# Kernel optimization log

Measured on AMD Instinct MI355X. Metric: run time of the kernel, lower is better.

Reference implementation:

```python
import jax, jax.numpy as jnp
import numpy as np

N_TOKENS = 100000
CUT = [0, 20000, 50000, 100000]  # cutoff_ends
D = 1024


def setup_inputs() -> dict:
    key = jax.random.key(0)
    ks = jax.random.split(key, 12)
    B, S = 2, 1024
    hidden = jax.random.normal(ks[0], (B, S, D), dtype=jnp.float32)
    target = jax.random.randint(ks[1], (B, S), 0, N_TOKENS, dtype=jnp.int64)
    s = 0.02
    # cluster 0 (shortlist) + cluster projection head
    w0 = jax.random.normal(ks[2], (20000, 1024), dtype=jnp.float32) * s
    b0 = jnp.zeros((20000,), jnp.float32)
    cluster_w = jax.random.normal(ks[3], (2, 1024), dtype=jnp.float32) * s  # n_clusters=2
    cluster_b = jnp.zeros((2,), jnp.float32)
    proj0 = jax.random.normal(ks[4], (1024, 1024), dtype=jnp.float32) * s  # d_proj x d_emb_0
    # tail cluster 1: d_emb_1 = 1024 // 4 = 256, vocab slice 20000..50000
    w1 = jax.random.normal(ks[5], (30000, 256), dtype=jnp.float32) * s
    b1 = jnp.zeros((30000,), jnp.float32)
    proj1 = jax.random.normal(ks[6], (1024, 256), dtype=jnp.float32) * s
    # tail cluster 2: d_emb_2 = 1024 // 16 = 64, vocab slice 50000..100000
    w2 = jax.random.normal(ks[7], (50000, 64), dtype=jnp.float32) * s
    b2 = jnp.zeros((50000,), jnp.float32)
    proj2 = jax.random.normal(ks[8], (1024, 64), dtype=jnp.float32) * s
    return {"hidden": hidden, "target": target,
            "w0": w0, "b0": b0, "cluster_w": cluster_w, "cluster_b": cluster_b, "proj0": proj0,
            "w1": w1, "b1": b1, "proj1": proj1,
            "w2": w2, "b2": b2, "proj2": proj2}


def reference(hidden, target, w0, b0, cluster_w, cluster_b, proj0,
              w1, b1, proj1, w2, b2, proj2):
    tgt_shape = target.shape
    h = hidden.reshape(-1, D)            # [N, d_proj]
    t = target.reshape(-1)               # [N]

    # head: shortlist logits + cluster logits, via low-rank projection
    head_w = jnp.concatenate([w0, cluster_w], axis=0)   # [20002, 1024]
    head_b = jnp.concatenate([b0, cluster_b], axis=0)
    head_logit = (h @ proj0) @ head_w.T + head_b        # [N, 20002]
    head_lp = jax.nn.log_softmax(head_logit, axis=1)

    nll = jnp.zeros(t.shape, h.dtype)

    # cluster 0 (shortlist): logprob is head_lp at the target id
    m0 = t < CUT[1]
    idx0 = jnp.clip(t, 0, CUT[1] - 1)
    lp0 = jnp.take_along_axis(head_lp, idx0[:, None], axis=1)[:, 0]
    nll = jnp.where(m0, -lp0, nll)

    # tail clusters. NOTE: faithful to original quirk head_logprob[:, -i]
    tails = [(CUT[1], CUT[2], w1, b1, proj1), (CUT[2], CUT[3], w2, b2, proj2)]
    for i, (left, right, w, b, p) in enumerate(tails, start=1):
        m = (t >= left) & (t < right)
        tail_logit = (h @ p) @ w.T + b                  # [N, right-left]
        tail_lp = jax.nn.log_softmax(tail_logit, axis=1)
        ti = jnp.clip(t - left, 0, right - left - 1)
        lp = head_lp[:, -i] + jnp.take_along_axis(tail_lp, ti[:, None], axis=1)[:, 0]
        nll = jnp.where(m, -lp, nll)

    return nll.reshape(tgt_shape)
```

## Files before the change

### kernel.cpp

```cpp
#include <hip/hip_runtime.h>
#include <cstdint>
#include <cstddef>

#define DEV static __device__ __forceinline__

typedef __attribute__((ext_vector_type(8))) short bf16x8_t;
typedef __attribute__((ext_vector_type(4))) float f32x4_t;

DEV unsigned short f2bf(float f) {
  union { float f; unsigned u; } v; v.f = f;
  unsigned r = v.u + 0x7fffu + ((v.u >> 16) & 1u);
  return (unsigned short)(r >> 16);
}

DEV void gl_lds16(const void* g, void* l) {
  __builtin_amdgcn_global_load_lds(
      (const __attribute__((address_space(1))) void*)g,
      (__attribute__((address_space(3))) void*)l,
      16, 0, 0);
}

__global__ __launch_bounds__(256)
void prep_k(const int* __restrict__ target,
            int* __restrict__ idx1, int* __restrict__ pos1,
            int* __restrict__ idx2, int* __restrict__ pos2,
            int* __restrict__ cnts,
            const float* __restrict__ p0, const float* __restrict__ p1,
            const float* __restrict__ p2, unsigned short* __restrict__ pAll,
            const float* __restrict__ s0, unsigned short* __restrict__ d0, int n0,
            const float* __restrict__ s1, unsigned short* __restrict__ d1, int n1,
            const float* __restrict__ s2, unsigned short* __restrict__ d2, int n2,
            const float* __restrict__ s3, unsigned short* __restrict__ d3, int n3,
            const float* __restrict__ s4, unsigned short* __restrict__ d4, int n4) {
  const int bid = blockIdx.x;
  const int tid = threadIdx.x;
  if (bid == 0) {
    __shared__ int c1, c2;
    if (tid == 0) { c1 = 0; c2 = 0; }
    __syncthreads();
    for (int i = tid; i < 2048; i += 256) {
      int t = target[i];
      if (t >= 20000 && t < 50000) {
        int p = atomicAdd(&c1, 1); idx1[p] = i; pos1[i] = p;
      } else if (t >= 50000) {
        int p = atomicAdd(&c2, 1); idx2[p] = i; pos2[i] = p;
      }
    }
    __syncthreads();
    if (tid == 0) { cnts[0] = c1; cnts[1] = c2; }
    return;
  }
  if (bid <= 1344) {
    __shared__ float tile[32][33];
    int b = bid - 1;
    const float* src; unsigned short* dst; int C, bx, by;
    if (b < 1024)      { src = p0; dst = pAll;               C = 1024; bx = b % 32; by = b / 32; }
    else if (b < 1280) { int q = b - 1024; src = p1; dst = pAll + 1024 * 1024; C = 256; bx = q % 8; by = q / 8; }
    else               { int q = b - 1280; src = p2; dst = pAll + 1280 * 1024; C = 64;  bx = q % 2; by = q / 2; }
    const int R = 1024;
    int tx = tid & 31, ty = tid >> 5;
    int c0 = bx * 32, r0 = by * 32;
    for (int yy = ty; yy < 32; yy += 8)
      tile[yy][tx] = src[(size_t)(r0 + yy) * C + (c0 + tx)];
    __syncthreads();
    for (int yy = ty; yy < 32; yy += 8)
      dst[(size_t)(c0 + yy) * R + (r0 + tx)] = f2bf(tile[tx][yy]);
    return;
  }
  int j = (bid - 1345) * 256 + tid;
  const float* s; unsigned short* d;
  if (j < n0) { s = s0; d = d0; }
  else { j -= n0;
    if (j < n1) { s = s1; d = d1; }
    else { j -= n1;
      if (j < n2) { s = s2; d = d2; }
      else { j -= n2;
        if (j < n3) { s = s3; d = d3; }
        else { j -= n3; if (j >= n4) return; s = s4; d = d4; }
      }
    }
  }
  float4 f = ((const float4*)s)[j];
  ushort4 o;
  o.x = f2bf(f.x); o.y = f2bf(f.y); o.z = f2bf(f.z); o.w = f2bf(f.w);
  ((ushort4*)d)[j] = o;
}

__global__ __launch_bounds__(256)
void proj_gemm_k(const unsigned short* __restrict__ A,
                 const unsigned short* __restrict__ W,
                 unsigned short* __restrict__ Cout) {
  __shared__ __align__(16) unsigned short As[128 * 32];
  __shared__ __align__(16) unsigned short Bs[128 * 32];
  const int K = 1024, V = 1344;
  const int tm = blockIdx.x, tn = blockIdx.y;
  const int m0 = tm * 128, n0 = tn * 128;
  const int tid = threadIdx.x, wid = tid >> 6, lane = tid & 63;
  const int quad = lane >> 4, l16 = lane & 15;
  const int wr = wid >> 1, wc = wid & 1;

  f32x4_t acc[4][4];
  const f32x4_t zero4 = {0.f, 0.f, 0.f, 0.f};
#pragma unroll
  for (int i = 0; i < 4; ++i)
#pragma unroll
    for (int j = 0; j < 4; ++j) acc[i][j] = zero4;

  const int srow = wid * 32 + (lane >> 2);
  const int skk  = (lane & 3) * 8;
  const unsigned short* Ap0 = A + (size_t)(m0 + srow) * K + skk;
  const unsigned short* Ap1 = A + (size_t)(m0 + srow + 16) * K + skk;
  int wrow0 = n0 + srow;      if (wrow0 > V - 1) wrow0 = V - 1;
  int wrow1 = n0 + srow + 16; if (wrow1 > V - 1) wrow1 = V - 1;
  const unsigned short* Wp0 = W + (size_t)wrow0 * K + skk;
  const unsigned short* Wp1 = W + (size_t)wrow1 * K + skk;
  unsigned short* Asw = As + wid * 1024;
  unsigned short* Bsw = Bs + wid * 1024;

  for (int k0 = 0; k0 < K; k0 += 32) {
    gl_lds16(Ap0, Asw);
    gl_lds16(Ap1, Asw + 512);
    gl_lds16(Wp0, Bsw);
    gl_lds16(Wp1, Bsw + 512);
    Ap0 += 32; Ap1 += 32; Wp0 += 32; Wp1 += 32;
    __syncthreads();
    bf16x8_t af[4], bfr[4];
#pragma unroll
    for (int i = 0; i < 4; ++i)
      af[i] = *(const bf16x8_t*)(As + (size_t)(wr * 64 + i * 16 + l16) * 32 + quad * 8);
#pragma unroll
    for (int j = 0; j < 4; ++j)
      bfr[j] = *(const bf16x8_t*)(Bs + (size_t)(wc * 64 + j * 16 + l16) * 32 + quad * 8);
#pragma unroll
    for (int i = 0; i < 4; ++i)
#pragma unroll
      for (int j = 0; j < 4; ++j)
        acc[i][j] = __builtin_amdgcn_mfma_f32_16x16x32_bf16(af[i], bfr[j], acc[i][j], 0, 0, 0);
    __syncthreads();
  }
#pragma unroll
  for (int i = 0; i < 4; ++i)
#pragma unroll
    for (int j = 0; j < 4; ++j) {
      const int n = n0 + wc * 64 + j * 16 + l16;
      if (n < V) {
#pragma unroll
        for (int r = 0; r < 4; ++r) {
          const int m = m0 + wr * 64 + i * 16 + quad * 4 + r;
          Cout[(size_t)m * V + n] = f2bf(acc[i][j][r]);
        }
      }
    }
}


#define SBAR()                                                                \
  __builtin_amdgcn_sched_barrier(0);                                          \
  __builtin_amdgcn_s_barrier();                                               \
  __builtin_amdgcn_sched_barrier(0)

#define LGKM0()                                                               \
  asm volatile("s_waitcnt lgkmcnt(0)" ::: "memory");                          \
  __builtin_amdgcn_sched_barrier(0)

#define STA(BUF, HALF, KT)                                                    \
  {                                                                           \
    const unsigned short* g_ = aB0 + (size_t)(HALF) * (128 * 1344) + (KT) * 64; \
    char* d_ = (char*)SA[BUF][HALF] + ldsw;                                   \
    gl_lds16(g_, d_);                                                         \
    gl_lds16(g_ + 64 * 1344, d_ + 8192);                                      \
  }

#define STB(BUF, HALF, KT)                                                    \
  {                                                                           \
    char* d_ = (char*)SB[BUF][HALF] + ldsw;                                   \
    gl_lds16(bP##HALF##0 + (KT) * 64, d_);                                    \
    gl_lds16(bP##HALF##1 + (KT) * 64, d_ + 8192);                             \
  }

#define MM16(mb, nb)                                                          \
  {                                                                           \
    _Pragma("unroll") for (int mi = 0; mi < 4; ++mi) {                        \
      _Pragma("unroll") for (int nj = 0; nj < 2; ++nj) {                      \
        acc[(mb) + mi][(nb) + nj] = __builtin_amdgcn_mfma_f32_16x16x32_bf16(  \
            Af[0][mi], Bf[(nb) / 2][0][nj], acc[(mb) + mi][(nb) + nj], 0, 0, 0); \
        acc[(mb) + mi][(nb) + nj] = __builtin_amdgcn_mfma_f32_16x16x32_bf16(  \
            Af[1][mi], Bf[(nb) / 2][1][nj], acc[(mb) + mi][(nb) + nj], 0, 0, 0); \
      }                                                                       \
    }                                                                         \
  }

#define PH(D_, E_, KTV)                                                       \
  {                                                                           \
    const int kt_ = (KTV);                                                    \
    const int t1_ = (kt_ + 1 > 15) ? 15 : (kt_ + 1);                          \
    const int t2_ = (kt_ + 2 > 15) ? 15 : (kt_ + 2);                          \
                   \
    _Pragma("unroll") for (int mi = 0; mi < 4; ++mi) {                        \
      Af[0][mi] = *(const bf16x8_t*)(pa##D_##a + mi * 2048);                  \
      Af[1][mi] = *(const bf16x8_t*)(pa##D_##b + mi * 2048);                  \
    }                                                                         \
    _Pragma("unroll") for (int nj = 0; nj < 2; ++nj) {                        \
      Bf[0][0][nj] = *(const bf16x8_t*)(pb##D_##a + nj * 2048);               \
      Bf[0][1][nj] = *(const bf16x8_t*)(pb##D_##b + nj * 2048);               \
    }                                                                         \
    STB(E_, 1, t1_);                                                          \
    SBAR();                                                                   \
    LGKM0();                                                                  \
    __builtin_amdgcn_s_setprio(1);                                            \
    MM16(0, 0);                                                               \
    __builtin_amdgcn_s_setprio(0);                                            \
                                            \
    _Pragma("unroll") for (int nj = 0; nj < 2; ++nj) {                        \
      Bf[1][0][nj] = *(const bf16x8_t*)(pb##D_##a + (2 + nj) * 2048);         \
      Bf[1][1][nj] = *(const bf16x8_t*)(pb##D_##b + (2 + nj) * 2048);         \
    }                                                                         \
    SBAR();                                                                   \
    STA(E_, 1, t1_);                                                          \
    SBAR();                                                                   \
    LGKM0();                                                                  \
    __builtin_amdgcn_s_setprio(1);                                            \
    MM16(0, 2);                                                               \
    __builtin_amdgcn_s_setprio(0);                                            \
       \
    _Pragma("unroll") for (int mi = 0; mi < 4; ++mi) {                        \
      Af[0][mi] = *(const bf16x8_t*)(pa##D_##a + (4 + mi) * 2048);            \
      Af[1][mi] = *(const bf16x8_t*)(pa##D_##b + (4 + mi) * 2048);            \
    }                                                                         \
    SBAR();                                                                   \
    STB(D_, 0, t2_);                                                          \
    SBAR();                                                                   \
    LGKM0();                                                                  \
    __builtin_amdgcn_s_setprio(1);                                            \
    MM16(4, 0);                                                               \
    __builtin_amdgcn_s_setprio(0);                                            \
    SBAR();                                                                   \
    STA(D_, 0, t2_);                                                          \
    SBAR();                                                                   \
    __builtin_amdgcn_s_setprio(1);                                            \
    MM16(4, 2);                                                               \
    __builtin_amdgcn_s_setprio(0);                                            \
    asm volatile("s_waitcnt vmcnt(4)" ::: "memory");                          \
    SBAR();                                                                   \
  }

__global__ __launch_bounds__(512, 2)
void head256_k(const unsigned short* __restrict__ Pall,
               const unsigned short* __restrict__ w0b,
               const float* __restrict__ b0, const float* __restrict__ cb,
               float* __restrict__ part0, float* __restrict__ g0,
               float* __restrict__ cg, const int* __restrict__ target) {
  __shared__ __align__(16) unsigned short SA[2][2][8192];
  __shared__ __align__(16) unsigned short SB[2][2][8192];

  const int V = 20002;
  const int bid = blockIdx.x;
  const int orig = (bid & 7) * 79 + (bid >> 3);
  const int mt = orig & 7, stripe = orig >> 3;
  const int m0 = mt * 256, n0 = stripe * 256;

  const int tid = threadIdx.x;
  const int wid = tid >> 6, lane = tid & 63;
  const int quad = lane >> 4, l16 = lane & 15;
  const int wr = wid >> 2, wc = wid & 3;

  const int r0  = tid >> 3;
  const int ibh = ((tid & 7) ^ (r0 & 7)) << 3;

  const unsigned short* aB0 = Pall + (size_t)(m0 + r0) * 1344 + ibh;
  int br00 = n0 + r0;            if (br00 > V - 1) br00 = V - 1;
  int br01 = n0 + r0 + 64;       if (br01 > V - 1) br01 = V - 1;
  int br10 = n0 + 128 + r0;      if (br10 > V - 1) br10 = V - 1;
  int br11 = n0 + 128 + r0 + 64; if (br11 > V - 1) br11 = V - 1;
  const unsigned short* bP00 = w0b + (size_t)br00 * 1024 + ibh;
  const unsigned short* bP01 = w0b + (size_t)br01 * 1024 + ibh;
  const unsigned short* bP10 = w0b + (size_t)br10 * 1024 + ibh;
  const unsigned short* bP11 = w0b + (size_t)br11 * 1024 + ibh;

  const int ldsw = wid * 1024;

  const int aoff0 = l16 * 128 + ((quad ^ (l16 & 3)) << 4) + (((l16 >> 2) & 1) << 6);
  const int aoff1 = aoff0 ^ 64;
  const char* pa0a = (const char*)SA[0][wr] + aoff0;
  const char* pa0b = (const char*)SA[0][wr] + aoff1;
  const char* pa1a = (const char*)SA[1][wr] + aoff0;
  const char* pa1b = (const char*)SA[1][wr] + aoff1;
  const char* pb0a = (const char*)SB[0][wc >> 1] + (wc & 1) * 8192 + aoff0;
  const char* pb0b = (const char*)SB[0][wc >> 1] + (wc & 1) * 8192 + aoff1;
  const char* pb1a = (const char*)SB[1][wc >> 1] + (wc & 1) * 8192 + aoff0;
  const char* pb1b = (const char*)SB[1][wc >> 1] + (wc & 1) * 8192 + aoff1;

  f32x4_t acc[8][4];
  const f32x4_t zero4 = {0.f, 0.f, 0.f, 0.f};
#pragma unroll
  for (int i = 0; i < 8; ++i)
#pragma unroll
    for (int j = 0; j < 4; ++j) acc[i][j] = zero4;

  bf16x8_t Af[2][4];
  bf16x8_t Bf[2][2][2];

  STB(0, 0, 0); STA(0, 0, 0); STB(0, 1, 0); STA(0, 1, 0);
  STB(1, 0, 1); STA(1, 0, 1);
  asm volatile("s_waitcnt vmcnt(4)" ::: "memory");
  SBAR();

#pragma unroll 1
  for (int ktp = 0; ktp < 8; ++ktp) {
    const int kt0 = 2 * ktp;
    PH(0, 1, kt0);
    PH(1, 0, kt0 + 1);
  }

  asm volatile("s_waitcnt vmcnt(0)" ::: "memory");
  SBAR();

  int nj[4]; float bj[4];
#pragma unroll
  for (int j = 0; j < 4; ++j) {
    nj[j] = n0 + wc * 64 + j * 16 + l16;
    bj[j] = (nj[j] < 20000) ? b0[nj[j]] : ((nj[j] < V) ? cb[nj[j] - 20000] : 0.f);
  }
  float* redf = (float*)&SA[0][0][0];
#pragma unroll
  for (int i = 0; i < 8; ++i) {
#pragma unroll
    for (int r = 0; r < 4; ++r) {
      const int rloc = i * 16 + quad * 4 + r;
      const int token = m0 + wr * 128 + rloc;
      float v[4], sum = 0.f;
#pragma unroll
      for (int j = 0; j < 4; ++j) {
        v[j] = acc[i][j][r] + bj[j];
        if (nj[j] < V) sum += __expf(v[j]);
      }
#pragma unroll
      for (int off = 1; off < 16; off <<= 1)
        sum += __shfl_xor(sum, off, 64);
      if (l16 == 0) redf[(wr * 4 + wc) * 128 + rloc] = sum;
      const int t = target[token];
      const int gi = (t < 19999) ? t : 19999;
#pragma unroll
      for (int j = 0; j < 4; ++j) {
        if (nj[j] == gi) g0[token] = v[j];
        if (nj[j] == 20000) cg[2 * token]     = v[j];
        if (nj[j] == 20001) cg[2 * token + 1] = v[j];
      }
    }
  }
  __syncthreads();
  if (tid < 256) {
    const int wrr = tid >> 7, rr = tid & 127;
    const float s = redf[(wrr * 4 + 0) * 128 + rr] + redf[(wrr * 4 + 1) * 128 + rr]
                  + redf[(wrr * 4 + 2) * 128 + rr] + redf[(wrr * 4 + 3) * 128 + rr];
    part0[(size_t)(m0 + tid) * 79 + stripe] = s;
  }
}

#undef PH
#undef MM16
#undef STA
#undef STB
#undef SBAR
#undef LGKM0

template <int KT>
__global__ __launch_bounds__(256, 1)
void tail_stripe_k(const unsigned short* __restrict__ A, int ldA,
                   const unsigned short* __restrict__ W,
                   const float* __restrict__ bias, int V, int ntiles,
                   const int* __restrict__ rowidx,
                   const int* __restrict__ cnt_ptr,
                   float* __restrict__ partials,
                   float* __restrict__ gathered,
                   const int* __restrict__ target, int glo) {
  constexpr int NC = KT / 32;
  __shared__ __align__(16) unsigned short Ws[NC][128 * 32];
  __shared__ __align__(16) unsigned short As[NC][128 * 32];
  __shared__ float red[2][128];

  const int tn = blockIdx.x, n0 = tn * 128;
  const int Meff = *cnt_ptr;
  const int tid = threadIdx.x, wid = tid >> 6, lane = tid & 63;
  const int quad = lane >> 4, l16 = lane & 15;
  const int wr = wid >> 1, wc = wid & 1;
  const int srow = wid * 32 + (lane >> 2);
  const int skk  = (lane & 3) * 8;

  int wrow0 = n0 + srow;      if (wrow0 > V - 1) wrow0 = V - 1;
  int wrow1 = n0 + srow + 16; if (wrow1 > V - 1) wrow1 = V - 1;
#pragma unroll
  for (int c = 0; c < NC; ++c) {
    gl_lds16(W + (size_t)wrow0 * KT + c * 32 + skk, Ws[c] + wid * 1024);
    gl_lds16(W + (size_t)wrow1 * KT + c * 32 + skk, Ws[c] + wid * 1024 + 512);
  }

  int nj[4]; float bj[4];
#pragma unroll
  for (int j = 0; j < 4; ++j) {
    nj[j] = n0 + wc * 64 + j * 16 + l16;
    bj[j] = (nj[j] < V) ? bias[nj[j]] : 0.f;
  }

  const int nm = (Meff + 127) >> 7;
  for (int m = 0; m < nm; ++m) {
    const int m0 = m * 128;
    int ar0 = m0 + srow;      if (ar0 > Meff - 1) ar0 = Meff - 1;
    int ar1 = m0 + srow + 16; if (ar1 > Meff - 1) ar1 = Meff - 1;
    ar0 = rowidx[ar0]; ar1 = rowidx[ar1];
#pragma unroll
    for (int c = 0; c < NC; ++c) {
      gl_lds16(A + (size_t)ar0 * ldA + c * 32 + skk, As[c] + wid * 1024);
      gl_lds16(A + (size_t)ar1 * ldA + c * 32 + skk, As[c] + wid * 1024 + 512);
    }
    __syncthreads();

    f32x4_t acc[4][4];
    const f32x4_t zero4 = {0.f, 0.f, 0.f, 0.f};
#pragma unroll
    for (int i = 0; i < 4; ++i)
#pragma unroll
      for (int j = 0; j < 4; ++j) acc[i][j] = zero4;
#pragma unroll
    for (int c = 0; c < NC; ++c) {
      bf16x8_t af[4], bfr[4];
#pragma unroll
      for (int i = 0; i < 4; ++i)
        af[i] = *(const bf16x8_t*)(As[c] + (size_t)(wr * 64 + i * 16 + l16) * 32 + quad * 8);
#pragma unroll
      for (int j = 0; j < 4; ++j)
        bfr[j] = *(const bf16x8_t*)(Ws[c] + (size_t)(wc * 64 + j * 16 + l16) * 32 + quad * 8);
#pragma unroll
      for (int i = 0; i < 4; ++i)
#pragma unroll
        for (int j = 0; j < 4; ++j)
          acc[i][j] = __builtin_amdgcn_mfma_f32_16x16x32_bf16(af[i], bfr[j], acc[i][j], 0, 0, 0);
    }

#pragma unroll
    for (int i = 0; i < 4; ++i) {
#pragma unroll
      for (int r = 0; r < 4; ++r) {
        const int row = wr * 64 + i * 16 + quad * 4 + r;
        const int gr = m0 + row;
        const int grc = (gr < Meff) ? gr : (Meff - 1);
        const int token = rowidx[grc];
        float v[4], sum = 0.f;
#pragma unroll
        for (int j = 0; j < 4; ++j) {
          v[j] = acc[i][j][r] + bj[j];
          if (nj[j] < V) sum += __expf(v[j]);
        }
#pragma unroll
        for (int off = 1; off < 16; off <<= 1)
          sum += __shfl_xor(sum, off, 64);
        if (l16 == 0) red[wc][row] = sum;
        const int gi = target[token] - glo;
#pragma unroll
        for (int j = 0; j < 4; ++j)
          if (nj[j] == gi) gathered[token] = v[j];
      }
    }
    __syncthreads();
    if (tid < 128 && (m0 + tid) < Meff)
      partials[(size_t)(m0 + tid) * ntiles + tn] = red[0][tid] + red[1][tid];
  }
}

__global__ __launch_bounds__(256)
void combine_k(const float* __restrict__ part0,
               const float* __restrict__ part1, int nt1,
               const float* __restrict__ part2, int nt2,
               const float* __restrict__ g0, const float* __restrict__ g1,
               const float* __restrict__ g2, const float* __restrict__ cg,
               const int* __restrict__ pos1, const int* __restrict__ pos2,
               const int* __restrict__ target, float* __restrict__ out) {
  const int w = threadIdx.x >> 6, lane = threadIdx.x & 63;
  const int token = blockIdx.x * 4 + w;
  const int t = target[token];

  float S = 0.f;
  for (int i = lane; i < 79; i += 64)
    S += part0[(size_t)token * 79 + i];
#pragma unroll
  for (int off = 1; off < 64; off <<= 1)
    S += __shfl_xor(S, off, 64);
  const float lse_head = __logf(S);

  float res;
  if (t < 20000) {
    res = lse_head - g0[token];
  } else {
    const float* pt; int nt; float gv, ch; int row;
    if (t < 50000) { pt = part1; nt = nt1; gv = g1[token]; ch = cg[2 * token + 1]; row = pos1[token]; }
    else           { pt = part2; nt = nt2; gv = g2[token]; ch = cg[2 * token];     row = pos2[token]; }
    float S2 = 0.f;
    for (int i = lane; i < nt; i += 64)
      S2 += pt[(size_t)row * nt + i];
#pragma unroll
    for (int off = 1; off < 64; off <<= 1)
      S2 += __shfl_xor(S2, off, 64);
    float lse_t = __logf(S2);
    res = -((ch - lse_head) + (gv - lse_t));
  }
  if (lane == 0) out[token] = res;
}

extern "C" void kernel_launch(void* const* d_in, const int* in_sizes, int n_in,
                              void* d_out, int out_size, void* d_ws, size_t ws_size,
                              hipStream_t stream) {
  (void)in_sizes; (void)n_in; (void)out_size; (void)ws_size;
  const float* hidden = (const float*)d_in[0];
  const int*   target = (const int*)d_in[1];
  const float* w0     = (const float*)d_in[2];
  const float* b0     = (const float*)d_in[3];
  const float* cw     = (const float*)d_in[4];
  const float* cb     = (const float*)d_in[5];
  const float* proj0  = (const float*)d_in[6];
  const float* w1     = (const float*)d_in[7];
  const float* b1     = (const float*)d_in[8];
  const float* proj1  = (const float*)d_in[9];
  const float* w2     = (const float*)d_in[10];
  const float* b2     = (const float*)d_in[11];
  const float* proj2  = (const float*)d_in[12];
  float* out = (float*)d_out;

  const int NT1 = 235, NT2 = 391;

  char* p = (char*)d_ws;
  auto alloc = [&](size_t bytes) {
    char* r = p; p += (bytes + 255) & ~(size_t)255; return r;
  };
  unsigned short* Hb   = (unsigned short*)alloc(2048ull * 1024 * 2);
  unsigned short* pAll = (unsigned short*)alloc(1344ull * 1024 * 2);
  unsigned short* w0b  = (unsigned short*)alloc(20002ull * 1024 * 2);
  unsigned short* w1b  = (unsigned short*)alloc(30000ull * 256 * 2);
  unsigned short* w2b  = (unsigned short*)alloc(50000ull * 64 * 2);
  unsigned short* Pall = (unsigned short*)alloc(2048ull * 1344 * 2);
  float* part0 = (float*)alloc(2048ull * 79 * 4);
  float* part1 = (float*)alloc(2048ull * NT1 * 4);
  float* part2 = (float*)alloc(2048ull * NT2 * 4);
  float* g0 = (float*)alloc(2048 * 4);
  float* g1 = (float*)alloc(2048 * 4);
  float* g2 = (float*)alloc(2048 * 4);
  float* cg = (float*)alloc(2048 * 2 * 4);
  int* idx1 = (int*)alloc(2048 * 4);
  int* pos1 = (int*)alloc(2048 * 4);
  int* idx2 = (int*)alloc(2048 * 4);
  int* pos2 = (int*)alloc(2048 * 4);
  int* cnts = (int*)alloc(2 * 4);

  const int c_h = 2048 * 1024 / 4, c_w0 = 20000 * 1024 / 4, c_cw = 2048 / 4,
            c_w1 = 30000 * 256 / 4, c_w2 = 50000 * 64 / 4;
  const int ctot = c_h + c_w0 + c_cw + c_w1 + c_w2;
  const int nb_cast = (ctot + 255) / 256;
  prep_k<<<1 + 1344 + nb_cast, 256, 0, stream>>>(
      target, idx1, pos1, idx2, pos2, cnts,
      proj0, proj1, proj2, pAll,
      hidden, Hb, c_h,
      w0, w0b, c_w0,
      cw, w0b + 20000ull * 1024, c_cw,
      w1, w1b, c_w1,
      w2, w2b, c_w2);

  proj_gemm_k<<<dim3(16, 11), 256, 0, stream>>>(Hb, pAll, Pall);

  head256_k<<<632, 512, 0, stream>>>(Pall, w0b, b0, cb, part0, g0, cg, target);

  tail_stripe_k<256><<<NT1, 256, 0, stream>>>(
      Pall + 1024, 1344, w1b, b1, 30000, NT1, idx1, cnts + 0,
      part1, g1, target, 20000);
  tail_stripe_k<64><<<NT2, 256, 0, stream>>>(
      Pall + 1280, 1344, w2b, b2, 50000, NT2, idx2, cnts + 1,
      part2, g2, target, 50000);

  combine_k<<<512, 256, 0, stream>>>(part0, part1, NT1, part2, NT2,
      g0, g1, g2, cg, pos1, pos2, target, out);
}
```

Baseline: 428.4 us.

## Make head GEMM persistent with atomic tile scheduler and prefetch-overlapped epilogue

```diff
diff --git a/kernel.cpp b/kernel.cpp
--- a/kernel.cpp
+++ b/kernel.cpp
@@ -47,7 +47,7 @@
       }
     }
     __syncthreads();
-    if (tid == 0) { cnts[0] = c1; cnts[1] = c2; }
+    if (tid == 0) { cnts[0] = c1; cnts[1] = c2; cnts[2] = 256; }
     return;
   }
   if (bid <= 1344) {
@@ -154,14 +154,8 @@
 }
 
 
-#define SBAR()                                                                \
-  __builtin_amdgcn_sched_barrier(0);                                          \
-  __builtin_amdgcn_s_barrier();                                               \
-  __builtin_amdgcn_sched_barrier(0)
-
-#define LGKM0()                                                               \
-  asm volatile("s_waitcnt lgkmcnt(0)" ::: "memory");                          \
-  __builtin_amdgcn_sched_barrier(0)
+#define SBAR() __builtin_amdgcn_s_barrier()
+#define LGKM0() asm volatile("s_waitcnt lgkmcnt(0)" ::: "memory")
 
 #define STA(BUF, HALF, KT)                                                    \
   {                                                                           \
@@ -195,7 +189,7 @@
     const int kt_ = (KTV);                                                    \
     const int t1_ = (kt_ + 1 > 15) ? 15 : (kt_ + 1);                          \
     const int t2_ = (kt_ + 2 > 15) ? 15 : (kt_ + 2);                          \
-                   \
+                                       \
     _Pragma("unroll") for (int mi = 0; mi < 4; ++mi) {                        \
       Af[0][mi] = *(const bf16x8_t*)(pa##D_##a + mi * 2048);                  \
       Af[1][mi] = *(const bf16x8_t*)(pa##D_##b + mi * 2048);                  \
@@ -205,60 +199,52 @@
       Bf[0][1][nj] = *(const bf16x8_t*)(pb##D_##b + nj * 2048);               \
     }                                                                         \
     STB(E_, 1, t1_);                                                          \
+    SBAR(); LGKM0();                                                          \
+    __builtin_amdgcn_s_setprio(1); MM16(0, 0); __builtin_amdgcn_s_setprio(0); \
     SBAR();                                                                   \
-    LGKM0();                                                                  \
-    __builtin_amdgcn_s_setprio(1);                                            \
-    MM16(0, 0);                                                               \
-    __builtin_amdgcn_s_setprio(0);                                            \
-                                            \
+                                               \
     _Pragma("unroll") for (int nj = 0; nj < 2; ++nj) {                        \
       Bf[1][0][nj] = *(const bf16x8_t*)(pb##D_##a + (2 + nj) * 2048);         \
       Bf[1][1][nj] = *(const bf16x8_t*)(pb##D_##b + (2 + nj) * 2048);         \
     }                                                                         \
+    STA(E_, 1, t1_);                                                          \
+    SBAR(); LGKM0();                                                          \
+    __builtin_amdgcn_s_setprio(1); MM16(0, 2); __builtin_amdgcn_s_setprio(0); \
     SBAR();                                                                   \
-    STA(E_, 1, t1_);                                                          \
-    SBAR();                                                                   \
-    LGKM0();                                                                  \
-    __builtin_amdgcn_s_setprio(1);                                            \
-    MM16(0, 2);                                                               \
-    __builtin_amdgcn_s_setprio(0);                                            \
-       \
+                                               \
     _Pragma("unroll") for (int mi = 0; mi < 4; ++mi) {                        \
       Af[0][mi] = *(const bf16x8_t*)(pa##D_##a + (4 + mi) * 2048);            \
       Af[1][mi] = *(const bf16x8_t*)(pa##D_##b + (4 + mi) * 2048);            \
     }                                                                         \
+    STB(D_, 0, t2_);                                                          \
+    SBAR(); LGKM0();                                                          \
+    __builtin_amdgcn_s_setprio(1); MM16(4, 0); __builtin_amdgcn_s_setprio(0); \
     SBAR();                                                                   \
-    STB(D_, 0, t2_);                                                          \
-    SBAR();                                                                   \
-    LGKM0();                                                                  \
-    __builtin_amdgcn_s_setprio(1);                                            \
-    MM16(4, 0);                                                               \
-    __builtin_amdgcn_s_setprio(0);                                            \
-    SBAR();                                                                   \
+                    \
     STA(D_, 0, t2_);                                                          \
     SBAR();                                                                   \
-    __builtin_amdgcn_s_setprio(1);                                            \
-    MM16(4, 2);                                                               \
-    __builtin_amdgcn_s_setprio(0);                                            \
+    __builtin_amdgcn_s_setprio(1); MM16(4, 2); __builtin_amdgcn_s_setprio(0); \
     asm volatile("s_waitcnt vmcnt(4)" ::: "memory");                          \
     SBAR();                                                                   \
   }
+
+#define PROLOGUE6()                                                           \
+  { STB(0, 0, 0); STA(0, 0, 0); STB(0, 1, 0); STA(0, 1, 0);                   \
+    STB(1, 0, 1); STA(1, 0, 1); }
 
 __global__ __launch_bounds__(512, 2)
 void head256_k(const unsigned short* __restrict__ Pall,
                const unsigned short* __restrict__ w0b,
                const float* __restrict__ b0, const float* __restrict__ cb,
                float* __restrict__ part0, float* __restrict__ g0,
-               float* __restrict__ cg, const int* __restrict__ target) {
+               float* __restrict__ cg, const int* __restrict__ target,
+               int* __restrict__ tilectr) {
   __shared__ __align__(16) unsigned short SA[2][2][8192];
   __shared__ __align__(16) unsigned short SB[2][2][8192];
-
-  const int V = 20002;
-  const int bid = blockIdx.x;
-  const int orig = (bid & 7) * 79 + (bid >> 3);
-  const int mt = orig & 7, stripe = orig >> 3;
-  const int m0 = mt * 256, n0 = stripe * 256;
-
+  __shared__ float redf2[1024];
+  __shared__ int nextS;
+
+  const int V = 20002, NTILE = 632;
   const int tid = threadIdx.x;
   const int wid = tid >> 6, lane = tid & 63;
   const int quad = lane >> 4, l16 = lane & 15;
@@ -266,17 +252,6 @@
 
   const int r0  = tid >> 3;
   const int ibh = ((tid & 7) ^ (r0 & 7)) << 3;
-
-  const unsigned short* aB0 = Pall + (size_t)(m0 + r0) * 1344 + ibh;
-  int br00 = n0 + r0;            if (br00 > V - 1) br00 = V - 1;
-  int br01 = n0 + r0 + 64;       if (br01 > V - 1) br01 = V - 1;
-  int br10 = n0 + 128 + r0;      if (br10 > V - 1) br10 = V - 1;
-  int br11 = n0 + 128 + r0 + 64; if (br11 > V - 1) br11 = V - 1;
-  const unsigned short* bP00 = w0b + (size_t)br00 * 1024 + ibh;
-  const unsigned short* bP01 = w0b + (size_t)br01 * 1024 + ibh;
-  const unsigned short* bP10 = w0b + (size_t)br10 * 1024 + ibh;
-  const unsigned short* bP11 = w0b + (size_t)br11 * 1024 + ibh;
-
   const int ldsw = wid * 1024;
 
   const int aoff0 = l16 * 128 + ((quad ^ (l16 & 3)) << 4) + (((l16 >> 2) & 1) << 6);
@@ -290,77 +265,116 @@
   const char* pb1a = (const char*)SB[1][wc >> 1] + (wc & 1) * 8192 + aoff0;
   const char* pb1b = (const char*)SB[1][wc >> 1] + (wc & 1) * 8192 + aoff1;
 
+  int m0, n0, stripe;
+  const unsigned short* aB0;
+  const unsigned short *bP00, *bP01, *bP10, *bP11;
+
+  int tile = blockIdx.x;
+#define DECODE(T)                                                             \
+  {                                                                           \
+    const int t_ = (T);                                                       \
+    stripe = t_ >> 3; m0 = (t_ & 7) * 256; n0 = stripe * 256;                 \
+    aB0 = Pall + (size_t)(m0 + r0) * 1344 + ibh;                              \
+    int q00 = n0 + r0;            if (q00 > V - 1) q00 = V - 1;               \
+    int q01 = n0 + r0 + 64;       if (q01 > V - 1) q01 = V - 1;               \
+    int q10 = n0 + 128 + r0;      if (q10 > V - 1) q10 = V - 1;               \
+    int q11 = n0 + 128 + r0 + 64; if (q11 > V - 1) q11 = V - 1;               \
+    bP00 = w0b + (size_t)q00 * 1024 + ibh;                                    \
+    bP01 = w0b + (size_t)q01 * 1024 + ibh;                                    \
+    bP10 = w0b + (size_t)q10 * 1024 + ibh;                                    \
+    bP11 = w0b + (size_t)q11 * 1024 + ibh;                                    \
+  }
+
+  DECODE(tile);
+  PROLOGUE6();
+  asm volatile("s_waitcnt vmcnt(4)" ::: "memory");
+  SBAR();
+
   f32x4_t acc[8][4];
-  const f32x4_t zero4 = {0.f, 0.f, 0.f, 0.f};
-#pragma unroll
-  for (int i = 0; i < 8; ++i)
-#pragma unroll
-    for (int j = 0; j < 4; ++j) acc[i][j] = zero4;
-
   bf16x8_t Af[2][4];
   bf16x8_t Bf[2][2][2];
-
-  STB(0, 0, 0); STA(0, 0, 0); STB(0, 1, 0); STA(0, 1, 0);
-  STB(1, 0, 1); STA(1, 0, 1);
-  asm volatile("s_waitcnt vmcnt(4)" ::: "memory");
-  SBAR();
+  const f32x4_t zero4 = {0.f, 0.f, 0.f, 0.f};
+
+  while (true) {
+#pragma unroll
+    for (int i = 0; i < 8; ++i)
+#pragma unroll
+      for (int j = 0; j < 4; ++j) acc[i][j] = zero4;
 
 #pragma unroll 1
-  for (int ktp = 0; ktp < 8; ++ktp) {
-    const int kt0 = 2 * ktp;
-    PH(0, 1, kt0);
-    PH(1, 0, kt0 + 1);
-  }
-
-  asm volatile("s_waitcnt vmcnt(0)" ::: "memory");
-  SBAR();
-
-  int nj[4]; float bj[4];
-#pragma unroll
-  for (int j = 0; j < 4; ++j) {
-    nj[j] = n0 + wc * 64 + j * 16 + l16;
-    bj[j] = (nj[j] < 20000) ? b0[nj[j]] : ((nj[j] < V) ? cb[nj[j] - 20000] : 0.f);
-  }
-  float* redf = (float*)&SA[0][0][0];
-#pragma unroll
-  for (int i = 0; i < 8; ++i) {
-#pragma unroll
-    for (int r = 0; r < 4; ++r) {
-      const int rloc = i * 16 + quad * 4 + r;
-      const int token = m0 + wr * 128 + rloc;
-      float v[4], sum = 0.f;
-#pragma unroll
-      for (int j = 0; j < 4; ++j) {
-        v[j] = acc[i][j][r] + bj[j];
-        if (nj[j] < V) sum += __expf(v[j]);
+    for (int ktp = 0; ktp < 8; ++ktp) {
+      const int kt0 = 2 * ktp;
+      PH(0, 1, kt0);
+      PH(1, 0, kt0 + 1);
+    }
+
+    if (tid == 0) nextS = atomicAdd(tilectr, 1);
+    asm volatile("s_waitcnt vmcnt(0) lgkmcnt(0)" ::: "memory");
+    SBAR();
+    const int next = nextS;
+    const bool more = (next < NTILE);
+
+    const int em0 = m0, estripe = stripe;
+    int nj[4]; float bj[4];
+#pragma unroll
+    for (int j = 0; j < 4; ++j) {
+      nj[j] = n0 + wc * 64 + j * 16 + l16;
+      bj[j] = (nj[j] < 20000) ? b0[nj[j]] : ((nj[j] < V) ? cb[nj[j] - 20000] : 0.f);
+    }
+
+    if (more) {
+      DECODE(next);
+      PROLOGUE6();
+    }
+
+#pragma unroll
+    for (int i = 0; i < 8; ++i) {
+#pragma unroll
+      for (int r = 0; r < 4; ++r) {
+        const int rloc = i * 16 + quad * 4 + r;
+        const int token = em0 + wr * 128 + rloc;
+        float v[4], sum = 0.f;
+#pragma unroll
+        for (int j = 0; j < 4; ++j) {
+          v[j] = acc[i][j][r] + bj[j];
+          if (nj[j] < V) sum += __expf(v[j]);
+        }
+#pragma unroll
+        for (int off = 1; off < 16; off <<= 1)
+          sum += __shfl_xor(sum, off, 64);
+        if (l16 == 0) redf2[(wr * 4 + wc) * 128 + rloc] = sum;
+        const int t = target[token];
+        const int gi = (t < 19999) ? t : 19999;
+#pragma unroll
+        for (int j = 0; j < 4; ++j) {
+          if (nj[j] == gi) g0[token] = v[j];
+          if (nj[j] == 20000) cg[2 * token]     = v[j];
+          if (nj[j] == 20001) cg[2 * token + 1] = v[j];
+        }
       }
-#pragma unroll
-      for (int off = 1; off < 16; off <<= 1)
-        sum += __shfl_xor(sum, off, 64);
-      if (l16 == 0) redf[(wr * 4 + wc) * 128 + rloc] = sum;
-      const int t = target[token];
-      const int gi = (t < 19999) ? t : 19999;
-#pragma unroll
-      for (int j = 0; j < 4; ++j) {
-        if (nj[j] == gi) g0[token] = v[j];
-        if (nj[j] == 20000) cg[2 * token]     = v[j];
-        if (nj[j] == 20001) cg[2 * token + 1] = v[j];
-      }
-    }
-  }
-  __syncthreads();
-  if (tid < 256) {
-    const int wrr = tid >> 7, rr = tid & 127;
-    const float s = redf[(wrr * 4 + 0) * 128 + rr] + redf[(wrr * 4 + 1) * 128 + rr]
-                  + redf[(wrr * 4 + 2) * 128 + rr] + redf[(wrr * 4 + 3) * 128 + rr];
-    part0[(size_t)(m0 + tid) * 79 + stripe] = s;
-  }
+    }
+    LGKM0();
+    SBAR();
+    if (tid < 256) {
+      const int wrr = tid >> 7, rr = tid & 127;
+      const float s = redf2[(wrr * 4 + 0) * 128 + rr] + redf2[(wrr * 4 + 1) * 128 + rr]
+                    + redf2[(wrr * 4 + 2) * 128 + rr] + redf2[(wrr * 4 + 3) * 128 + rr];
+      part0[(size_t)(em0 + tid) * 79 + estripe] = s;
+    }
+    if (!more) return;
+
+    asm volatile("s_waitcnt vmcnt(4)" ::: "memory");
+    SBAR();
+    tile = next;
+  }
+#undef DECODE
 }
 
 #undef PH
 #undef MM16
 #undef STA
 #undef STB
+#undef PROLOGUE6
 #undef SBAR
 #undef LGKM0
 
@@ -548,7 +562,7 @@
   int* pos1 = (int*)alloc(2048 * 4);
   int* idx2 = (int*)alloc(2048 * 4);
   int* pos2 = (int*)alloc(2048 * 4);
-  int* cnts = (int*)alloc(2 * 4);
+  int* cnts = (int*)alloc(4 * 4);
 
   const int c_h = 2048 * 1024 / 4, c_w0 = 20000 * 1024 / 4, c_cw = 2048 / 4,
             c_w1 = 30000 * 256 / 4, c_w2 = 50000 * 64 / 4;
@@ -565,7 +579,8 @@
 
   proj_gemm_k<<<dim3(16, 11), 256, 0, stream>>>(Hb, pAll, Pall);
 
-  head256_k<<<632, 512, 0, stream>>>(Pall, w0b, b0, cb, part0, g0, cg, target);
+  head256_k<<<256, 512, 0, stream>>>(Pall, w0b, b0, cb, part0, g0, cg, target,
+                                     cnts + 2);
 
   tail_stripe_k<256><<<NT1, 256, 0, stream>>>(
       Pall + 1024, 1344, w1b, b1, 30000, NT1, idx1, cnts + 0,
```

After: 434.7 us. No clear change (+1.5%).

## Reschedule head GEMM pipeline with B-fragment double buffering and fewer barriers

Applied to the files above, without the earlier changes.

```diff
diff --git a/kernel.cpp b/kernel.cpp
--- a/kernel.cpp
+++ b/kernel.cpp
@@ -154,14 +154,7 @@
 }
 
 
-#define SBAR()                                                                \
-  __builtin_amdgcn_sched_barrier(0);                                          \
-  __builtin_amdgcn_s_barrier();                                               \
-  __builtin_amdgcn_sched_barrier(0)
-
-#define LGKM0()                                                               \
-  asm volatile("s_waitcnt lgkmcnt(0)" ::: "memory");                          \
-  __builtin_amdgcn_sched_barrier(0)
+#define SBAR() __builtin_amdgcn_s_barrier()
 
 #define STA(BUF, HALF, KT)                                                    \
   {                                                                           \
@@ -178,14 +171,14 @@
     gl_lds16(bP##HALF##1 + (KT) * 64, d_ + 8192);                             \
   }
 
-#define MM16(mb, nb)                                                          \
+#define MMQ(mb, nb, BB)                                                       \
   {                                                                           \
     _Pragma("unroll") for (int mi = 0; mi < 4; ++mi) {                        \
       _Pragma("unroll") for (int nj = 0; nj < 2; ++nj) {                      \
         acc[(mb) + mi][(nb) + nj] = __builtin_amdgcn_mfma_f32_16x16x32_bf16(  \
-            Af[0][mi], Bf[(nb) / 2][0][nj], acc[(mb) + mi][(nb) + nj], 0, 0, 0); \
+            Af[0][mi], BB[0][nj], acc[(mb) + mi][(nb) + nj], 0, 0, 0);        \
         acc[(mb) + mi][(nb) + nj] = __builtin_amdgcn_mfma_f32_16x16x32_bf16(  \
-            Af[1][mi], Bf[(nb) / 2][1][nj], acc[(mb) + mi][(nb) + nj], 0, 0, 0); \
+            Af[1][mi], BB[1][nj], acc[(mb) + mi][(nb) + nj], 0, 0, 0);        \
       }                                                                       \
     }                                                                         \
   }
@@ -195,54 +188,44 @@
     const int kt_ = (KTV);                                                    \
     const int t1_ = (kt_ + 1 > 15) ? 15 : (kt_ + 1);                          \
     const int t2_ = (kt_ + 2 > 15) ? 15 : (kt_ + 2);                          \
-                   \
+              \
     _Pragma("unroll") for (int mi = 0; mi < 4; ++mi) {                        \
       Af[0][mi] = *(const bf16x8_t*)(pa##D_##a + mi * 2048);                  \
       Af[1][mi] = *(const bf16x8_t*)(pa##D_##b + mi * 2048);                  \
     }                                                                         \
     _Pragma("unroll") for (int nj = 0; nj < 2; ++nj) {                        \
-      Bf[0][0][nj] = *(const bf16x8_t*)(pb##D_##a + nj * 2048);               \
-      Bf[0][1][nj] = *(const bf16x8_t*)(pb##D_##b + nj * 2048);               \
+      Bh[0][nj] = *(const bf16x8_t*)(pb##D_##a + (2 + nj) * 2048);            \
+      Bh[1][nj] = *(const bf16x8_t*)(pb##D_##b + (2 + nj) * 2048);            \
     }                                                                         \
     STB(E_, 1, t1_);                                                          \
+    __builtin_amdgcn_s_setprio(1); MMQ(0, 0, Bl); __builtin_amdgcn_s_setprio(0); \
     SBAR();                                                                   \
-    LGKM0();                                                                  \
-    __builtin_amdgcn_s_setprio(1);                                            \
-    MM16(0, 0);                                                               \
-    __builtin_amdgcn_s_setprio(0);                                            \
-                                            \
-    _Pragma("unroll") for (int nj = 0; nj < 2; ++nj) {                        \
-      Bf[1][0][nj] = *(const bf16x8_t*)(pb##D_##a + (2 + nj) * 2048);         \
-      Bf[1][1][nj] = *(const bf16x8_t*)(pb##D_##b + (2 + nj) * 2048);         \
-    }                                                                         \
-    SBAR();                                                                   \
-    STA(E_, 1, t1_);                                                          \
-    SBAR();                                                                   \
-    LGKM0();                                                                  \
-    __builtin_amdgcn_s_setprio(1);                                            \
-    MM16(0, 2);                                                               \
-    __builtin_amdgcn_s_setprio(0);                                            \
-       \
+              \
+    __builtin_amdgcn_s_setprio(1); MMQ(0, 2, Bh); __builtin_amdgcn_s_setprio(0); \
     _Pragma("unroll") for (int mi = 0; mi < 4; ++mi) {                        \
       Af[0][mi] = *(const bf16x8_t*)(pa##D_##a + (4 + mi) * 2048);            \
       Af[1][mi] = *(const bf16x8_t*)(pa##D_##b + (4 + mi) * 2048);            \
     }                                                                         \
+    STA(E_, 1, t1_);                                                          \
     SBAR();                                                                   \
+               \
     STB(D_, 0, t2_);                                                          \
+    __builtin_amdgcn_s_setprio(1); MMQ(4, 0, Bl); __builtin_amdgcn_s_setprio(0); \
+    asm volatile("s_waitcnt vmcnt(2)" ::: "memory");                          \
     SBAR();                                                                   \
-    LGKM0();                                                                  \
-    __builtin_amdgcn_s_setprio(1);                                            \
-    MM16(4, 0);                                                               \
-    __builtin_amdgcn_s_setprio(0);                                            \
+           \
+    STA(D_, 0, t2_);                                                          \
+    _Pragma("unroll") for (int nj = 0; nj < 2; ++nj) {                        \
+      Bl[0][nj] = *(const bf16x8_t*)(pb##E_##a + nj * 2048);                  \
+      Bl[1][nj] = *(const bf16x8_t*)(pb##E_##b + nj * 2048);                  \
+    }                                                                         \
+    __builtin_amdgcn_s_setprio(1); MMQ(4, 2, Bh); __builtin_amdgcn_s_setprio(0); \
     SBAR();                                                                   \
-    STA(D_, 0, t2_);                                                          \
-    SBAR();                                                                   \
-    __builtin_amdgcn_s_setprio(1);                                            \
-    MM16(4, 2);                                                               \
-    __builtin_amdgcn_s_setprio(0);                                            \
-    asm volatile("s_waitcnt vmcnt(4)" ::: "memory");                          \
-    SBAR();                                                                   \
-  }
+  }
+
+#define PROLOGUE6()                                                           \
+  { STB(0, 0, 0); STA(0, 0, 0); STB(0, 1, 0); STA(0, 1, 0);                   \
+    STB(1, 0, 1); STA(1, 0, 1); }
 
 __global__ __launch_bounds__(512, 2)
 void head256_k(const unsigned short* __restrict__ Pall,
@@ -298,12 +281,17 @@
     for (int j = 0; j < 4; ++j) acc[i][j] = zero4;
 
   bf16x8_t Af[2][4];
-  bf16x8_t Bf[2][2][2];
-
-  STB(0, 0, 0); STA(0, 0, 0); STB(0, 1, 0); STA(0, 1, 0);
-  STB(1, 0, 1); STA(1, 0, 1);
+  bf16x8_t Bl[2][2];
+  bf16x8_t Bh[2][2];
+
+  PROLOGUE6();
   asm volatile("s_waitcnt vmcnt(4)" ::: "memory");
   SBAR();
+#pragma unroll
+  for (int nj = 0; nj < 2; ++nj) {
+    Bl[0][nj] = *(const bf16x8_t*)(pb0a + nj * 2048);
+    Bl[1][nj] = *(const bf16x8_t*)(pb0b + nj * 2048);
+  }
 
 #pragma unroll 1
   for (int ktp = 0; ktp < 8; ++ktp) {
@@ -312,7 +300,7 @@
     PH(1, 0, kt0 + 1);
   }
 
-  asm volatile("s_waitcnt vmcnt(0)" ::: "memory");
+  asm volatile("s_waitcnt vmcnt(0) lgkmcnt(0)" ::: "memory");
   SBAR();
 
   int nj[4]; float bj[4];
@@ -358,11 +346,11 @@
 }
 
 #undef PH
-#undef MM16
+#undef MMQ
 #undef STA
 #undef STB
+#undef PROLOGUE6
 #undef SBAR
-#undef LGKM0
 
 template <int KT>
 __global__ __launch_bounds__(256, 1)
```

Result: no change. 425.4 us (-0.7%).
